# Optimization experiments

Hardware: AMD Instinct MI355X
Metric: run time of the kernel (lower is better)

Reference implementation:

```python
import jax, jax.numpy as jnp
import numpy as np

EPS = 1e-5
OFFSET_SCALE = 1.0
KPTS = 9   # 3x3 deformable kernel
GROUP = 1  # in_dim // out_dim


def _bn(x, g, b, m, v):
    # eval-mode BatchNorm2d on (B,C,H,W)
    s = g / jnp.sqrt(v + EPS)
    return x * s[None, :, None, None] + (b - m * s)[None, :, None, None]


def _dcnv4_core(value, offset, mask, offset_scale):
    # value: (B,H,W,G,Cg); offset: (B,H,W,G,K,2) as (dx,dy); mask: (B,H,W,G,K)
    B, H, W, G, Cg = value.shape
    K = mask.shape[-1]
    dt = value.dtype
    ky = jnp.repeat(jnp.arange(3) - 1, 3).astype(dt)
    kx = jnp.tile(jnp.arange(3) - 1, 3).astype(dt)
    grid = jnp.stack([kx, ky], -1)                                   # (K,2)
    base = jnp.stack(jnp.meshgrid(jnp.arange(W, dtype=dt),
                                  jnp.arange(H, dtype=dt),
                                  indexing='xy'), -1)                # (H,W,2) = (x,y)
    loc = base[None, :, :, None, None, :] + (grid + offset) * offset_scale  # (B,H,W,G,K,2)
    px, py = loc[..., 0], loc[..., 1]
    x0 = jnp.floor(px); y0 = jnp.floor(py)
    fx = px - x0; fy = py - y0
    vflat = value.transpose(0, 3, 1, 2, 4).reshape(B, G, H * W, Cg)
    out = jnp.zeros((B, G, H * W, Cg), dt)
    corners = ((0.0, 0.0, (1 - fx) * (1 - fy)), (1.0, 0.0, fx * (1 - fy)),
               (0.0, 1.0, (1 - fx) * fy), (1.0, 1.0, fx * fy))
    for dx, dy, wgt in corners:
        xi = x0 + dx; yi = y0 + dy
        valid = ((xi >= 0) & (xi < W) & (yi >= 0) & (yi < H)).astype(dt)
        idx = (jnp.clip(yi, 0, W and H - 1) * W + jnp.clip(xi, 0, W - 1)).astype(jnp.int32)
        idx = idx.transpose(0, 3, 1, 2, 4).reshape(B, G, H * W * K)
        v = jnp.take_along_axis(vflat, idx[..., None], axis=2).reshape(B, G, H * W, K, Cg)
        w = (wgt * valid * mask).transpose(0, 3, 1, 2, 4).reshape(B, G, H * W, K)
        out = out + jnp.einsum('bgsk,bgskc->bgsc', w, v)
    return out.reshape(B, G, H, W, Cg).transpose(0, 2, 3, 1, 4).reshape(B, H, W, G * Cg)


def setup_inputs() -> dict:
    key = jax.random.key(0)
    B, C, H, W = 8, 128, 64, 64
    C_OUT = 128
    OM = ((GROUP * KPTS * 3 + 7) // 8) * 8  # 32, offset_mask padded width
    ks = jax.random.split(key, 16)
    f = jnp.float32
    sc = 1.0 / np.sqrt(C).astype(np.float32)
    return {
        'x': jax.random.normal(ks[0], (B, C, H, W), f),
        'bn1_g': jax.random.uniform(ks[1], (C,), f, 0.5, 1.5),
        'bn1_b': jax.random.normal(ks[2], (C,), f) * 0.1,
        'bn1_m': jax.random.normal(ks[3], (C,), f) * 0.1,
        'bn1_v': jax.random.uniform(ks[4], (C,), f, 0.5, 1.5),
        'w_pw0': jax.random.normal(ks[5], (C, C), f) * sc,
        'w_vp': jax.random.normal(ks[6], (C, C), f) * sc,
        'b_vp': jnp.zeros((C,), f),
        'w_om': jax.random.normal(ks[7], (C, OM), f) * 0.01,
        'b_om': jnp.zeros((OM,), f),
        'w_op': jax.random.normal(ks[8], (C, C), f) * sc,
        'bn2_g': jax.random.uniform(ks[9], (C,), f, 0.5, 1.5),
        'bn2_b': jax.random.normal(ks[10], (C,), f) * 0.1,
        'bn2_m': jax.random.normal(ks[11], (C,), f) * 0.1,
        'bn2_v': jax.random.uniform(ks[12], (C,), f, 0.5, 1.5),
        'w_pw1': jax.random.normal(ks[13], (C_OUT, C), f) * sc,
    }


def reference(x, bn1_g, bn1_b, bn1_m, bn1_v, w_pw0, w_vp, b_vp, w_om, b_om, w_op,
              bn2_g, bn2_b, bn2_m, bn2_v, w_pw1):
    x = _bn(x, bn1_g, bn1_b, bn1_m, bn1_v)
    x = jnp.einsum('bchw,oc->bohw', x, w_pw0)
    B, C, H, W = x.shape
    x = x.reshape(B, H * W, C)  # raw reshape (faithful to torch .reshape, NOT a permute)
    G, K = GROUP, KPTS
    Cg = C // G
    value = (x @ w_vp + b_vp).reshape(B, H, W, G, Cg)
    om = (x @ w_om + b_om)[..., :G * K * 3].reshape(B, H, W, G, K, 3)
    out = _dcnv4_core(value, om[..., :2], om[..., 2], OFFSET_SCALE)
    out = out.reshape(B, H * W, C) @ w_op
    x = out.reshape(B, C, H, W)  # raw reshape back
    x = _bn(x, bn2_g, bn2_b, bn2_m, bn2_v)
    x = jnp.einsum('bchw,oc->bohw', x, w_pw1)
    return x
```

## Files before the change

### kernel.cpp

```cpp
#include <hip/hip_runtime.h>

#define HW 4096
#define PADU 136
typedef unsigned short ushort;
typedef __attribute__((ext_vector_type(8))) short short8;
typedef __attribute__((ext_vector_type(4))) float f32x4;

__device__ __forceinline__ ushort bf_rne(float f) {
  unsigned u = __float_as_uint(f);
  unsigned r = (u + 0x7fffu + ((u >> 16) & 1u)) >> 16;
  return (ushort)r;
}
__device__ __forceinline__ void split2(float f, ushort& hi, ushort& lo) {
  ushort h = bf_rne(f);
  float hf = __uint_as_float((unsigned)h << 16);
  hi = h;
  lo = bf_rne(f - hf);
}

__global__ __launch_bounds__(256) void prep(
    const float* __restrict__ g1, const float* __restrict__ be1,
    const float* __restrict__ m1, const float* __restrict__ v1,
    const float* __restrict__ w0,
    const float* __restrict__ g2, const float* __restrict__ be2,
    const float* __restrict__ m2, const float* __restrict__ v2,
    const float* __restrict__ w1,
    const float* __restrict__ wvp, const float* __restrict__ wom,
    const float* __restrict__ wop,
    ushort* __restrict__ W0h, ushort* __restrict__ W0l, float* __restrict__ b0,
    ushort* __restrict__ W1h, ushort* __restrict__ W1l, float* __restrict__ b1,
    ushort* __restrict__ vph, ushort* __restrict__ vpl,
    ushort* __restrict__ oph, ushort* __restrict__ opl,
    ushort* __restrict__ omh, ushort* __restrict__ oml)
{
  const int t = threadIdx.x;
// ... 35 lines not shown
      #pragma unroll
      for (int j = 0; j < 16; ++j) s += part[t >> 4][j];
      bb[o] = s;
    }
  } else if (role < 32) {
    const int rr = role & 7;
    const float* srcM = (role < 24) ? wvp : wop;
    ushort* dh = (role < 24) ? vph : oph;
    ushort* dl = (role < 24) ? vpl : opl;
    const int n = (rr << 4) + (t >> 4);
    const int kl = t & 15;
    #pragma unroll
    for (int j = 0; j < 8; ++j) {
      const int k = (kl << 3) + j;
      ushort hi, lo;
      split2(srcM[k * 128 + n], hi, lo);
      dh[n * 128 + k] = hi;
      dl[n * 128 + k] = lo;
    }
  } else {
    const int n = ((role - 32) << 4) + (t >> 4);
    const int kl = t & 15;
    #pragma unroll
    for (int j = 0; j < 8; ++j) {
      const int k = (kl << 3) + j;
      ushort hi, lo;
      split2(wom[k * 32 + n], hi, lo);
      omh[n * 128 + k] = hi;
      oml[n * 128 + k] = lo;
    }
  }
}

__global__ __launch_bounds__(512, 2) void fused_x_valom(
    const float* __restrict__ x,
    const ushort* __restrict__ W0h, const ushort* __restrict__ W0l,
    const float* __restrict__ b0,
    const ushort* __restrict__ vph, const ushort* __restrict__ vpl,
    const float* __restrict__ bvp, const float* __restrict__ bom,
    float* __restrict__ value, float* __restrict__ omb)
{
  __shared__ __align__(16) char smem[151552];
  __shared__ float b0_s[128], b2_s[160];
  ushort (*Wh_s)[128][32] = (ushort(*)[128][32])(smem);
  ushort (*Wl_s)[128][32] = (ushort(*)[128][32])(smem + 32768);
  float  (*Xf)[128][33]   = (float(*)[128][33])(smem + 65536);
  ushort (*Yh)[PADU]      = (ushort(*)[PADU])(smem);
  ushort (*Yl)[PADU]      = (ushort(*)[PADU])(smem + 34816);
  ushort (*Vh_s)[160][32] = (ushort(*)[160][32])(smem + 69632);
  ushort (*Vl_s)[160][32] = (ushort(*)[160][32])(smem + 110592);

  const int t = threadIdx.x;
  const int cb = blockIdx.x;
  const int b = blockIdx.y;
  const int hwBase = cb << 7;
  const size_t xbase = (size_t)b * (size_t)(128 * HW);
  if (t < 128) b0_s[t] = b0[t];
  if (t < 160) b2_s[t] = (t < 128) ? bvp[t] : bom[t - 128];
  const int lane = t & 63, w = t >> 6;
  const int col = lane & 15, quad = lane >> 4;
  const f32x4 z = {0.f, 0.f, 0.f, 0.f};

  uint4 vregH[5], vregL[5];
  #pragma unroll
  for (int ii = 0; ii < 5; ++ii) {
    const int i = (ii << 9) + t;
    const int kc = i / 640;
    const int r2 = i - kc * 640;
    const int n = r2 >> 2, q8 = (r2 & 3) << 3;
    vregH[ii] = *(const uint4*)&vph[n * 128 + (kc << 5) + q8];
    vregL[ii] = *(const uint4*)&vpl[n * 128 + (kc << 5) + q8];
  }

  {
    const int o = t >> 2, q8 = (t & 3) << 3;
    #pragma unroll
    for (int kc = 0; kc < 4; ++kc) {
      *(uint4*)&Wh_s[kc][o][q8] = *(const uint4*)&W0h[o * 128 + (kc << 5) + q8];
      *(uint4*)&Wl_s[kc][o][q8] = *(const uint4*)&W0l[o * 128 + (kc << 5) + q8];
    }
  }
  {
    float4 xr4[8];
    #pragma unroll
    for (int i = 0; i < 8; ++i) {
      const int idx8 = (i << 9) + t;
      xr4[i] = *(const float4*)&x[xbase + (size_t)(idx8 >> 5) * HW + hwBase + ((idx8 & 31) << 2)];
    }
    #pragma unroll
    for (int i = 0; i < 8; ++i) {
      const int idx8 = (i << 9) + t;
      const int ch = idx8 >> 5, j4 = (idx8 & 31) << 2;
      Xf[ch >> 5][j4 + 0][ch & 31] = xr4[i].x;
      Xf[ch >> 5][j4 + 1][ch & 31] = xr4[i].y;
      Xf[ch >> 5][j4 + 2][ch & 31] = xr4[i].z;
      Xf[ch >> 5][j4 + 3][ch & 31] = xr4[i].w;
    }
  }
  __syncthreads();

  f32x4 acc1[8];
  #pragma unroll
  for (int f = 0; f < 8; ++f) acc1[f] = z;

  #pragma unroll 1
  for (int kc = 0; kc < 4; ++kc) {
    union { ushort u[8]; short8 v; } bh, bl;
    {
      const float* xr = Xf[kc][(w << 4) + col] + (quad << 3);
      #pragma unroll
      for (int j = 0; j < 8; ++j) split2(xr[j], bh.u[j], bl.u[j]);
    }
    #pragma unroll
    for (int f = 0; f < 8; ++f) {
      const int row = (f << 4) + col;
      const short8 aH = *(const short8*)&Wh_s[kc][row][quad << 3];
      const short8 aL = *(const short8*)&Wl_s[kc][row][quad << 3];
      acc1[f] = __builtin_amdgcn_mfma_f32_16x16x32_bf16(aH, bh.v, acc1[f], 0, 0, 0);
      acc1[f] = __builtin_amdgcn_mfma_f32_16x16x32_bf16(aH, bl.v, acc1[f], 0, 0, 0);
      acc1[f] = __builtin_amdgcn_mfma_f32_16x16x32_bf16(aL, bh.v, acc1[f], 0, 0, 0);
    }
  }
  __syncthreads();

  #pragma unroll
  for (int ii = 0; ii < 5; ++ii) {
    const int i = (ii << 9) + t;
    const int kc = i / 640;
    const int r2 = i - kc * 640;
    const int n = r2 >> 2, q8 = (r2 & 3) << 3;
    *(uint4*)&Vh_s[kc][n][q8] = vregH[ii];
    *(uint4*)&Vl_s[kc][n][q8] = vregL[ii];
  }
  #pragma unroll
  for (int f = 0; f < 8; ++f)
    #pragma unroll
    for (int r = 0; r < 4; ++r) {
      const int o = (f << 4) + (quad << 2) + r;
      const int j = (w << 4) + col;
      ushort hi, lo;
      split2(acc1[f][r] + b0_s[o], hi, lo);
      Yh[o][j] = hi;
      Yl[o][j] = lo;
    }
  __syncthreads();

  const int wm2 = (w & 3) << 5;
  const int wn2 = (w >> 2) * 80;
  f32x4 acc2[2][5];
  #pragma unroll
  for (int i = 0; i < 2; ++i)
    #pragma unroll
    for (int j = 0; j < 5; ++j) acc2[i][j] = z;

  #pragma unroll 1
  for (int j2 = 0; j2 < 4; ++j2) {
    short8 aH[2], aL[2];
    #pragma unroll
    for (int f2 = 0; f2 < 2; ++f2) {
      const int row = wm2 + (f2 << 4) + col;
      aH[f2] = *(const short8*)&Yh[row][(j2 << 5) + (quad << 3)];
      aL[f2] = *(const short8*)&Yl[row][(j2 << 5) + (quad << 3)];
    }
    #pragma unroll
    for (int g2 = 0; g2 < 5; ++g2) {
      const int n = wn2 + (g2 << 4) + col;
      const short8 vh = *(const short8*)&Vh_s[j2][n][quad << 3];
      const short8 vl = *(const short8*)&Vl_s[j2][n][quad << 3];
      #pragma unroll
      for (int f2 = 0; f2 < 2; ++f2) {
        acc2[f2][g2] = __builtin_amdgcn_mfma_f32_16x16x32_bf16(aH[f2], vh, acc2[f2][g2], 0, 0, 0);
        acc2[f2][g2] = __builtin_amdgcn_mfma_f32_16x16x32_bf16(aH[f2], vl, acc2[f2][g2], 0, 0, 0);
        acc2[f2][g2] = __builtin_amdgcn_mfma_f32_16x16x32_bf16(aL[f2], vh, acc2[f2][g2], 0, 0, 0);
      }
    }
  }
  #pragma unroll
  for (int f2 = 0; f2 < 2; ++f2)
    #pragma unroll
    for (int r = 0; r < 4; ++r) {
      const int m = wm2 + (f2 << 4) + (quad << 2) + r;
      const size_t gRow = (size_t)b * HW + (size_t)m * 32 + cb;
      #pragma unroll
      for (int g2 = 0; g2 < 5; ++g2) {
        const int n = wn2 + (g2 << 4) + col;
        const float v = acc2[f2][g2][r] + b2_s[n];
        if (n < 128) value[gRow * 128 + n] = v;
        else         omb[gRow * 32 + (n - 128)] = v;
      }
    }
}

__global__ __launch_bounds__(512, 2) void fused_sample_op_out(
    const float* __restrict__ value, const float* __restrict__ omb,
    const ushort* __restrict__ oph, const ushort* __restrict__ opl,
    const ushort* __restrict__ W1h, const ushort* __restrict__ W1l,
    const float* __restrict__ b1, float* __restrict__ out)
{
  __shared__ __align__(16) char smem[147456];
  __shared__ float b1_s[128];
  ushort (*Afh)[128][32]  = (ushort(*)[128][32])(smem);
  ushort (*Afl)[128][32]  = (ushort(*)[128][32])(smem + 32768);
  ushort (*Bh)[128][32]   = (ushort(*)[128][32])(smem + 65536);
  ushort (*Bl)[128][32]   = (ushort(*)[128][32])(smem + 98304);
  float  (*oms)[32]       = (float(*)[32])(smem + 131072);
  ushort (*Yh)[PADU]      = (ushort(*)[PADU])(smem);
  ushort (*Yl)[PADU]      = (ushort(*)[PADU])(smem + 34816);
  ushort (*W1h_)[128][32] = (ushort(*)[128][32])(smem + 69632);
  ushort (*W1l_)[128][32] = (ushort(*)[128][32])(smem + 102400);

  const int t = threadIdx.x;
  const int blk = blockIdx.x;
  const int b = blk & 7;
  const int cb = blk >> 3;
  if (t < 128) b1_s[t] = b1[t];
  const int lane = t & 63, w = t >> 6;
  const int col = lane & 15, quad = lane >> 4;
  const f32x4 z = {0.f, 0.f, 0.f, 0.f};

  {
    const int m0 = t >> 2, j8 = (t & 3) << 3;
    const size_t orow = ((size_t)b * HW + m0 * 32 + cb) * 32;
    *(float4*)&oms[m0][j8]     = *(const float4*)&omb[orow + j8];
    *(float4*)&oms[m0][j8 + 4] = *(const float4*)&omb[orow + j8 + 4];
  }
  #pragma unroll
  for (int i = 0; i < 4; ++i) {
    const int idx = (i << 9) + t;
    const int kc = idx >> 9, n = (idx >> 2) & 127, q8 = (idx & 3) << 3;
    *(uint4*)&Bh[kc][n][q8] = *(const uint4*)&oph[n * 128 + (kc << 5) + q8];
    *(uint4*)&Bl[kc][n][q8] = *(const uint4*)&opl[n * 128 + (kc << 5) + q8];
  }
  __syncthreads();

  {
    const int xhalf = lane >> 5;
    const int c4 = (lane & 31) << 2;
    const float* vb = value + (size_t)b * (size_t)(HW * 128) + c4;
    const int kcw = (lane & 31) >> 3;
    const int cow = (lane & 7) << 2;
    #pragma unroll 1
    for (int tt = 0; tt < 16; ++tt) {
      const int m = (w << 4) + tt;
      const int s = m * 32 + cb;
      const float fw = (float)(s & 63), fh = (float)(s >> 6);
      const float* omp = oms[m];
      float a0 = 0.f, a1 = 0.f, a2 = 0.f, a3 = 0.f;
      #pragma unroll
      for (int k = 0; k < 9; ++k) {
        const float dx = omp[k * 3 + 0];
        const float dy = omp[k * 3 + 1];
        const float mw = omp[k * 3 + 2];
        const float px = fw + (float)(k % 3 - 1) + dx;
        const float py = fh + (float)(k / 3 - 1) + dy;
        const float x0f = floorf(px), y0f = floorf(py);
        const float fx = px - x0f, fy = py - y0f;
        const int ix = (int)x0f + xhalf;
        const int iy = (int)y0f;
        const float wxm = (xhalf ? fx : 1.f - fx) * mw *
                          ((ix >= 0 && ix < 64) ? 1.f : 0.f);
        const int xc = min(max(ix, 0), 63);
        const int yc0 = min(max(iy, 0), 63);
        const int yc1 = min(max(iy + 1, 0), 63);
        const float w0 = wxm * (1.f - fy) * ((iy >= 0 && iy < 64) ? 1.f : 0.f);
        const float w1 = wxm * fy * ((iy + 1 >= 0 && iy + 1 < 64) ? 1.f : 0.f);
        const float4 v0 = *(const float4*)&vb[(size_t)((yc0 << 6) + xc) * 128];
        const float4 v1 = *(const float4*)&vb[(size_t)((yc1 << 6) + xc) * 128];
        a0 = fmaf(w0, v0.x, a0); a1 = fmaf(w0, v0.y, a1);
        a2 = fmaf(w0, v0.z, a2); a3 = fmaf(w0, v0.w, a3);
        a0 = fmaf(w1, v1.x, a0); a1 = fmaf(w1, v1.y, a1);
        a2 = fmaf(w1, v1.z, a2); a3 = fmaf(w1, v1.w, a3);
      }
      a0 += __shfl_xor(a0, 32); a1 += __shfl_xor(a1, 32);
      a2 += __shfl_xor(a2, 32); a3 += __shfl_xor(a3, 32);
      if (!xhalf) {
        ushort h0, l0, h1, l1, h2, l2, h3, l3;
        split2(a0, h0, l0); split2(a1, h1, l1);
        split2(a2, h2, l2); split2(a3, h3, l3);
        uint2 uh, ul;
        uh.x = (unsigned)h0 | ((unsigned)h1 << 16);
        uh.y = (unsigned)h2 | ((unsigned)h3 << 16);
        ul.x = (unsigned)l0 | ((unsigned)l1 << 16);
        ul.y = (unsigned)l2 | ((unsigned)l3 << 16);
        *(uint2*)&Afh[kcw][m][cow] = uh;
        *(uint2*)&Afl[kcw][m][cow] = ul;
      }
    }
  }
  __syncthreads();

  const int wm1 = (w & 1) << 6, wn1 = (w >> 1) << 5;
  f32x4 acc1[4][2];
  #pragma unroll
  for (int i = 0; i < 4; ++i) { acc1[i][0] = z; acc1[i][1] = z; }

  #pragma unroll 1
  for (int kc = 0; kc < 4; ++kc) {
    short8 aH[4], aL[4];
    #pragma unroll
    for (int f = 0; f < 4; ++f) {
      const int row = wm1 + (f << 4) + col;
      aH[f] = *(const short8*)&Afh[kc][row][quad << 3];
      aL[f] = *(const short8*)&Afl[kc][row][quad << 3];
    }
    #pragma unroll
    for (int g = 0; g < 2; ++g) {
      const int n = wn1 + (g << 4) + col;
      const short8 bh = *(const short8*)&Bh[kc][n][quad << 3];
      const short8 bl = *(const short8*)&Bl[kc][n][quad << 3];
      #pragma unroll
      for (int f = 0; f < 4; ++f) {
        acc1[f][g] = __builtin_amdgcn_mfma_f32_16x16x32_bf16(aH[f], bh, acc1[f][g], 0, 0, 0);
        acc1[f][g] = __builtin_amdgcn_mfma_f32_16x16x32_bf16(aH[f], bl, acc1[f][g], 0, 0, 0);
        acc1[f][g] = __builtin_amdgcn_mfma_f32_16x16x32_bf16(aL[f], bh, acc1[f][g], 0, 0, 0);
      }
    }
  }
  __syncthreads();

  #pragma unroll
  for (int i = 0; i < 4; ++i) {
    const int n = t >> 2, q8 = (t & 3) << 3;
    *(uint4*)&W1h_[i][n][q8] = *(const uint4*)&W1h[n * 128 + (i << 5) + q8];
    *(uint4*)&W1l_[i][n][q8] = *(const uint4*)&W1l[n * 128 + (i << 5) + q8];
  }
  #pragma unroll
  for (int f = 0; f < 4; ++f)
    #pragma unroll
    for (int g = 0; g < 2; ++g)
      #pragma unroll
      for (int r = 0; r < 4; ++r) {
        const int ch = wm1 + (f << 4) + (quad << 2) + r;
        const int j  = wn1 + (g << 4) + col;
        ushort hi, lo;
        split2(acc1[f][g][r], hi, lo);
        Yh[j][ch] = hi;
        Yl[j][ch] = lo;
      }
  __syncthreads();

  const int wm2 = (w & 1) << 6, wn2 = (w >> 1) << 5;
  f32x4 acc2[4][2];
  #pragma unroll
  for (int i = 0; i < 4; ++i) { acc2[i][0] = z; acc2[i][1] = z; }

  #pragma unroll 1
  for (int j2 = 0; j2 < 4; ++j2) {
    short8 aH[4], aL[4];
    #pragma unroll
    for (int f2 = 0; f2 < 4; ++f2) {
      const int row = wm2 + (f2 << 4) + col;
      aH[f2] = *(const short8*)&W1h_[j2][row][quad << 3];
      aL[f2] = *(const short8*)&W1l_[j2][row][quad << 3];
    }
    #pragma unroll
    for (int g2 = 0; g2 < 2; ++g2) {
      const int j = wn2 + (g2 << 4) + col;
      const short8 bh = *(const short8*)&Yh[j][(j2 << 5) + (quad << 3)];
      const short8 bl = *(const short8*)&Yl[j][(j2 << 5) + (quad << 3)];
      #pragma unroll
      for (int f2 = 0; f2 < 4; ++f2) {
        acc2[f2][g2] = __builtin_amdgcn_mfma_f32_16x16x32_bf16(aH[f2], bh, acc2[f2][g2], 0, 0, 0);
        acc2[f2][g2] = __builtin_amdgcn_mfma_f32_16x16x32_bf16(aH[f2], bl, acc2[f2][g2], 0, 0, 0);
        acc2[f2][g2] = __builtin_amdgcn_mfma_f32_16x16x32_bf16(aL[f2], bh, acc2[f2][g2], 0, 0, 0);
      }
    }
  }
  const size_t obase = (size_t)b * (size_t)(128 * HW) + ((size_t)cb << 7);
  #pragma unroll
  for (int f2 = 0; f2 < 4; ++f2)
    #pragma unroll
    for (int r = 0; r < 4; ++r) {
      const int o = wm2 + (f2 << 4) + (quad << 2) + r;
      #pragma unroll
      for (int g2 = 0; g2 < 2; ++g2) {
        const int j = wn2 + (g2 << 4) + col;
        out[obase + (size_t)o * HW + j] = acc2[f2][g2][r] + b1_s[o];
      }
    }
}

extern "C" void kernel_launch(void* const* d_in, const int* in_sizes, int n_in,
                              void* d_out, int out_size, void* d_ws, size_t ws_size,
                              hipStream_t stream)
{
  const float* x    = (const float*)d_in[0];
  const float* g1   = (const float*)d_in[1];
  const float* be1  = (const float*)d_in[2];
  const float* m1   = (const float*)d_in[3];
  const float* v1   = (const float*)d_in[4];
  const float* wpw0 = (const float*)d_in[5];
  const float* wvp  = (const float*)d_in[6];
  const float* bvp  = (const float*)d_in[7];
  const float* womW = (const float*)d_in[8];
  const float* bom  = (const float*)d_in[9];
  const float* wop  = (const float*)d_in[10];
  const float* g2   = (const float*)d_in[11];
  const float* be2  = (const float*)d_in[12];
  const float* m2   = (const float*)d_in[13];
  const float* v2   = (const float*)d_in[14];
  const float* wpw1 = (const float*)d_in[15];

  char* ws = (char*)d_ws;
  float*  value = (float*) (ws + 0);
  float*  omb   = (float*) (ws + 16777216);
  size_t o = 20971520;
  ushort* W0h = (ushort*)(ws + o); o += 32768;
  ushort* W0l = (ushort*)(ws + o); o += 32768;
  ushort* W1h = (ushort*)(ws + o); o += 32768;
  ushort* W1l = (ushort*)(ws + o); o += 32768;
  ushort* vph = (ushort*)(ws + o); o += 40960;
  ushort* vpl = (ushort*)(ws + o); o += 40960;
  ushort* oph = (ushort*)(ws + o); o += 32768;
  ushort* opl = (ushort*)(ws + o); o += 32768;
  float*  b0  = (float*)(ws + o);  o += 512;
  float*  b1  = (float*)(ws + o);
  ushort* omh = vph + 128 * 128;
  ushort* oml = vpl + 128 * 128;

  prep<<<34, 256, 0, stream>>>(g1, be1, m1, v1, wpw0, g2, be2, m2, v2, wpw1,
                               wvp, womW, wop,
                               W0h, W0l, b0, W1h, W1l, b1,
                               vph, vpl, oph, opl, omh, oml);
  fused_x_valom<<<dim3(32, 8), 512, 0, stream>>>(x, W0h, W0l, b0, vph, vpl,
                                                 bvp, bom, value, omb);
  fused_sample_op_out<<<dim3(256), 512, 0, stream>>>(value, omb, oph, opl,
                                                     W1h, W1l, b1, (float*)d_out);
}
```

Baseline: 154.2 us.

## Merge projection and sampling kernels into one cooperative launch with grid sync

```diff
diff --git a/kernel.cpp b/kernel.cpp
--- a/kernel.cpp
+++ b/kernel.cpp
@@ -1,4 +1,5 @@
 #include <hip/hip_runtime.h>
+#include <hip/hip_cooperative_groups.h>
 
 #define HW 4096
 #define PADU 136
@@ -102,352 +103,348 @@
   }
 }
 
-__global__ __launch_bounds__(512, 2) void fused_x_valom(
+__global__ __launch_bounds__(512, 2) void fused_all(
     const float* __restrict__ x,
     const ushort* __restrict__ W0h, const ushort* __restrict__ W0l,
     const float* __restrict__ b0,
     const ushort* __restrict__ vph, const ushort* __restrict__ vpl,
     const float* __restrict__ bvp, const float* __restrict__ bom,
-    float* __restrict__ value, float* __restrict__ omb)
-{
-  __shared__ __align__(16) char smem[151552];
-  __shared__ float b0_s[128], b2_s[160];
-  ushort (*Wh_s)[128][32] = (ushort(*)[128][32])(smem);
-  ushort (*Wl_s)[128][32] = (ushort(*)[128][32])(smem + 32768);
-  float  (*Xf)[128][33]   = (float(*)[128][33])(smem + 65536);
-  ushort (*Yh)[PADU]      = (ushort(*)[PADU])(smem);
-  ushort (*Yl)[PADU]      = (ushort(*)[PADU])(smem + 34816);
-  ushort (*Vh_s)[160][32] = (ushort(*)[160][32])(smem + 69632);
-  ushort (*Vl_s)[160][32] = (ushort(*)[160][32])(smem + 110592);
-
-  const int t = threadIdx.x;
-  const int cb = blockIdx.x;
-  const int b = blockIdx.y;
-  const int hwBase = cb << 7;
-  const size_t xbase = (size_t)b * (size_t)(128 * HW);
-  if (t < 128) b0_s[t] = b0[t];
-  if (t < 160) b2_s[t] = (t < 128) ? bvp[t] : bom[t - 128];
-  const int lane = t & 63, w = t >> 6;
-  const int col = lane & 15, quad = lane >> 4;
-  const f32x4 z = {0.f, 0.f, 0.f, 0.f};
-
-  uint4 vregH[5], vregL[5];
-  #pragma unroll
-  for (int ii = 0; ii < 5; ++ii) {
-    const int i = (ii << 9) + t;
-    const int kc = i / 640;
-    const int r2 = i - kc * 640;
-    const int n = r2 >> 2, q8 = (r2 & 3) << 3;
-    vregH[ii] = *(const uint4*)&vph[n * 128 + (kc << 5) + q8];
-    vregL[ii] = *(const uint4*)&vpl[n * 128 + (kc << 5) + q8];
-  }
-
-  {
-    const int o = t >> 2, q8 = (t & 3) << 3;
-    #pragma unroll
-    for (int kc = 0; kc < 4; ++kc) {
-      *(uint4*)&Wh_s[kc][o][q8] = *(const uint4*)&W0h[o * 128 + (kc << 5) + q8];
-      *(uint4*)&Wl_s[kc][o][q8] = *(const uint4*)&W0l[o * 128 + (kc << 5) + q8];
-    }
-  }
-  {
-    float4 xr4[8];
-    #pragma unroll
-    for (int i = 0; i < 8; ++i) {
-      const int idx8 = (i << 9) + t;
-      xr4[i] = *(const float4*)&x[xbase + (size_t)(idx8 >> 5) * HW + hwBase + ((idx8 & 31) << 2)];
-    }
-    #pragma unroll
-    for (int i = 0; i < 8; ++i) {
-      const int idx8 = (i << 9) + t;
-      const int ch = idx8 >> 5, j4 = (idx8 & 31) << 2;
-      Xf[ch >> 5][j4 + 0][ch & 31] = xr4[i].x;
-      Xf[ch >> 5][j4 + 1][ch & 31] = xr4[i].y;
-      Xf[ch >> 5][j4 + 2][ch & 31] = xr4[i].z;
-      Xf[ch >> 5][j4 + 3][ch & 31] = xr4[i].w;
-    }
-  }
-  __syncthreads();
-
-  f32x4 acc1[8];
-  #pragma unroll
-  for (int f = 0; f < 8; ++f) acc1[f] = z;
-
-  #pragma unroll 1
-  for (int kc = 0; kc < 4; ++kc) {
-    union { ushort u[8]; short8 v; } bh, bl;
-    {
-      const float* xr = Xf[kc][(w << 4) + col] + (quad << 3);
-      #pragma unroll
-      for (int j = 0; j < 8; ++j) split2(xr[j], bh.u[j], bl.u[j]);
-    }
-    #pragma unroll
-    for (int f = 0; f < 8; ++f) {
-      const int row = (f << 4) + col;
-      const short8 aH = *(const short8*)&Wh_s[kc][row][quad << 3];
-      const short8 aL = *(const short8*)&Wl_s[kc][row][quad << 3];
-      acc1[f] = __builtin_amdgcn_mfma_f32_16x16x32_bf16(aH, bh.v, acc1[f], 0, 0, 0);
-      acc1[f] = __builtin_amdgcn_mfma_f32_16x16x32_bf16(aH, bl.v, acc1[f], 0, 0, 0);
-      acc1[f] = __builtin_amdgcn_mfma_f32_16x16x32_bf16(aL, bh.v, acc1[f], 0, 0, 0);
-    }
-  }
-  __syncthreads();
-
-  #pragma unroll
-  for (int ii = 0; ii < 5; ++ii) {
-    const int i = (ii << 9) + t;
-    const int kc = i / 640;
-    const int r2 = i - kc * 640;
-    const int n = r2 >> 2, q8 = (r2 & 3) << 3;
-    *(uint4*)&Vh_s[kc][n][q8] = vregH[ii];
-    *(uint4*)&Vl_s[kc][n][q8] = vregL[ii];
-  }
-  #pragma unroll
-  for (int f = 0; f < 8; ++f)
-    #pragma unroll
-    for (int r = 0; r < 4; ++r) {
-      const int o = (f << 4) + (quad << 2) + r;
-      const int j = (w << 4) + col;
-      ushort hi, lo;
-      split2(acc1[f][r] + b0_s[o], hi, lo);
-      Yh[o][j] = hi;
-      Yl[o][j] = lo;
-    }
-  __syncthreads();
-
-  const int wm2 = (w & 3) << 5;
-  const int wn2 = (w >> 2) * 80;
-  f32x4 acc2[2][5];
-  #pragma unroll
-  for (int i = 0; i < 2; ++i)
-    #pragma unroll
-    for (int j = 0; j < 5; ++j) acc2[i][j] = z;
-
-  #pragma unroll 1
-  for (int j2 = 0; j2 < 4; ++j2) {
-    short8 aH[2], aL[2];
-    #pragma unroll
-    for (int f2 = 0; f2 < 2; ++f2) {
-      const int row = wm2 + (f2 << 4) + col;
-      aH[f2] = *(const short8*)&Yh[row][(j2 << 5) + (quad << 3)];
-      aL[f2] = *(const short8*)&Yl[row][(j2 << 5) + (quad << 3)];
-    }
-    #pragma unroll
-    for (int g2 = 0; g2 < 5; ++g2) {
-      const int n = wn2 + (g2 << 4) + col;
-      const short8 vh = *(const short8*)&Vh_s[j2][n][quad << 3];
-      const short8 vl = *(const short8*)&Vl_s[j2][n][quad << 3];
-      #pragma unroll
-      for (int f2 = 0; f2 < 2; ++f2) {
-        acc2[f2][g2] = __builtin_amdgcn_mfma_f32_16x16x32_bf16(aH[f2], vh, acc2[f2][g2], 0, 0, 0);
-        acc2[f2][g2] = __builtin_amdgcn_mfma_f32_16x16x32_bf16(aH[f2], vl, acc2[f2][g2], 0, 0, 0);
-        acc2[f2][g2] = __builtin_amdgcn_mfma_f32_16x16x32_bf16(aL[f2], vh, acc2[f2][g2], 0, 0, 0);
-      }
-    }
-  }
-  #pragma unroll
-  for (int f2 = 0; f2 < 2; ++f2)
-    #pragma unroll
-    for (int r = 0; r < 4; ++r) {
-      const int m = wm2 + (f2 << 4) + (quad << 2) + r;
-      const size_t gRow = (size_t)b * HW + (size_t)m * 32 + cb;
-      #pragma unroll
-      for (int g2 = 0; g2 < 5; ++g2) {
-        const int n = wn2 + (g2 << 4) + col;
-        const float v = acc2[f2][g2][r] + b2_s[n];
-        if (n < 128) value[gRow * 128 + n] = v;
-        else         omb[gRow * 32 + (n - 128)] = v;
-      }
-    }
-}
-
-__global__ __launch_bounds__(512, 2) void fused_sample_op_out(
-    const float* __restrict__ value, const float* __restrict__ omb,
+    float* __restrict__ value, float* __restrict__ omb,
     const ushort* __restrict__ oph, const ushort* __restrict__ opl,
     const ushort* __restrict__ W1h, const ushort* __restrict__ W1l,
     const float* __restrict__ b1, float* __restrict__ out)
 {
-  __shared__ __align__(16) char smem[147456];
-  __shared__ float b1_s[128];
-  ushort (*Afh)[128][32]  = (ushort(*)[128][32])(smem);
-  ushort (*Afl)[128][32]  = (ushort(*)[128][32])(smem + 32768);
-  ushort (*Bh)[128][32]   = (ushort(*)[128][32])(smem + 65536);
-  ushort (*Bl)[128][32]   = (ushort(*)[128][32])(smem + 98304);
-  float  (*oms)[32]       = (float(*)[32])(smem + 131072);
-  ushort (*Yh)[PADU]      = (ushort(*)[PADU])(smem);
-  ushort (*Yl)[PADU]      = (ushort(*)[PADU])(smem + 34816);
-  ushort (*W1h_)[128][32] = (ushort(*)[128][32])(smem + 69632);
-  ushort (*W1l_)[128][32] = (ushort(*)[128][32])(smem + 102400);
+  __shared__ __align__(16) char smem[151552];
+  __shared__ float b0_s[128], b2_s[160], b1_s[128];
 
   const int t = threadIdx.x;
   const int blk = blockIdx.x;
   const int b = blk & 7;
   const int cb = blk >> 3;
-  if (t < 128) b1_s[t] = b1[t];
   const int lane = t & 63, w = t >> 6;
   const int col = lane & 15, quad = lane >> 4;
   const f32x4 z = {0.f, 0.f, 0.f, 0.f};
 
   {
-    const int m0 = t >> 2, j8 = (t & 3) << 3;
-    const size_t orow = ((size_t)b * HW + m0 * 32 + cb) * 32;
-    *(float4*)&oms[m0][j8]     = *(const float4*)&omb[orow + j8];
-    *(float4*)&oms[m0][j8 + 4] = *(const float4*)&omb[orow + j8 + 4];
+    ushort (*Wh_s)[128][32] = (ushort(*)[128][32])(smem);
+    ushort (*Wl_s)[128][32] = (ushort(*)[128][32])(smem + 32768);
+    float  (*Xf)[128][33]   = (float(*)[128][33])(smem + 65536);
+    ushort (*Yh)[PADU]      = (ushort(*)[PADU])(smem);
+    ushort (*Yl)[PADU]      = (ushort(*)[PADU])(smem + 34816);
+    ushort (*Vh_s)[160][32] = (ushort(*)[160][32])(smem + 69632);
+    ushort (*Vl_s)[160][32] = (ushort(*)[160][32])(smem + 110592);
+
+    const int hwBase = cb << 7;
+    const size_t xbase = (size_t)b * (size_t)(128 * HW);
+    if (t < 128) b0_s[t] = b0[t];
+    if (t < 160) b2_s[t] = (t < 128) ? bvp[t] : bom[t - 128];
+    if (t < 128) b1_s[t] = b1[t];
+
+    uint4 vregH[5], vregL[5];
+    #pragma unroll
+    for (int ii = 0; ii < 5; ++ii) {
+      const int i = (ii << 9) + t;
+      const int kc = i / 640;
+      const int r2 = i - kc * 640;
+      const int n = r2 >> 2, q8 = (r2 & 3) << 3;
+      vregH[ii] = *(const uint4*)&vph[n * 128 + (kc << 5) + q8];
+      vregL[ii] = *(const uint4*)&vpl[n * 128 + (kc << 5) + q8];
+    }
+
+    {
+      const int o = t >> 2, q8 = (t & 3) << 3;
+      #pragma unroll
+      for (int kc = 0; kc < 4; ++kc) {
+        *(uint4*)&Wh_s[kc][o][q8] = *(const uint4*)&W0h[o * 128 + (kc << 5) + q8];
+        *(uint4*)&Wl_s[kc][o][q8] = *(const uint4*)&W0l[o * 128 + (kc << 5) + q8];
+      }
+    }
+    {
+      float4 xr4[8];
+      #pragma unroll
+      for (int i = 0; i < 8; ++i) {
+        const int idx8 = (i << 9) + t;
+        xr4[i] = *(const float4*)&x[xbase + (size_t)(idx8 >> 5) * HW + hwBase + ((idx8 & 31) << 2)];
+      }
+      #pragma unroll
+      for (int i = 0; i < 8; ++i) {
+        const int idx8 = (i << 9) + t;
+        const int ch = idx8 >> 5, j4 = (idx8 & 31) << 2;
+        Xf[ch >> 5][j4 + 0][ch & 31] = xr4[i].x;
+        Xf[ch >> 5][j4 + 1][ch & 31] = xr4[i].y;
+        Xf[ch >> 5][j4 + 2][ch & 31] = xr4[i].z;
+        Xf[ch >> 5][j4 + 3][ch & 31] = xr4[i].w;
+      }
+    }
+    __syncthreads();
+
+    f32x4 acc1[8];
+    #pragma unroll
+    for (int f = 0; f < 8; ++f) acc1[f] = z;
+
+    #pragma unroll 1
+    for (int kc = 0; kc < 4; ++kc) {
+      union { ushort u[8]; short8 v; } bh, bl;
+      {
+        const float* xr = Xf[kc][(w << 4) + col] + (quad << 3);
+        #pragma unroll
+        for (int j = 0; j < 8; ++j) split2(xr[j], bh.u[j], bl.u[j]);
+      }
+      #pragma unroll
+      for (int f = 0; f < 8; ++f) {
+        const int row = (f << 4) + col;
+        const short8 aH = *(const short8*)&Wh_s[kc][row][quad << 3];
+        const short8 aL = *(const short8*)&Wl_s[kc][row][quad << 3];
+        acc1[f] = __builtin_amdgcn_mfma_f32_16x16x32_bf16(aH, bh.v, acc1[f], 0, 0, 0);
+        acc1[f] = __builtin_amdgcn_mfma_f32_16x16x32_bf16(aH, bl.v, acc1[f], 0, 0, 0);
+        acc1[f] = __builtin_amdgcn_mfma_f32_16x16x32_bf16(aL, bh.v, acc1[f], 0, 0, 0);
+      }
+    }
+    __syncthreads();
+
+    #pragma unroll
+    for (int ii = 0; ii < 5; ++ii) {
+      const int i = (ii << 9) + t;
+      const int kc = i / 640;
+      const int r2 = i - kc * 640;
+      const int n = r2 >> 2, q8 = (r2 & 3) << 3;
+      *(uint4*)&Vh_s[kc][n][q8] = vregH[ii];
+      *(uint4*)&Vl_s[kc][n][q8] = vregL[ii];
+    }
+    #pragma unroll
+    for (int f = 0; f < 8; ++f)
+      #pragma unroll
+      for (int r = 0; r < 4; ++r) {
+        const int o = (f << 4) + (quad << 2) + r;
+        const int j = (w << 4) + col;
+        ushort hi, lo;
+        split2(acc1[f][r] + b0_s[o], hi, lo);
+        Yh[o][j] = hi;
+        Yl[o][j] = lo;
+      }
+    __syncthreads();
+
+    const int wm2 = (w & 3) << 5;
+    const int wn2 = (w >> 2) * 80;
+    f32x4 acc2[2][5];
+    #pragma unroll
+    for (int i = 0; i < 2; ++i)
+      #pragma unroll
+      for (int j = 0; j < 5; ++j) acc2[i][j] = z;
+
+    #pragma unroll 1
+    for (int j2 = 0; j2 < 4; ++j2) {
+      short8 aH[2], aL[2];
+      #pragma unroll
+      for (int f2 = 0; f2 < 2; ++f2) {
+        const int row = wm2 + (f2 << 4) + col;
+        aH[f2] = *(const short8*)&Yh[row][(j2 << 5) + (quad << 3)];
+        aL[f2] = *(const short8*)&Yl[row][(j2 << 5) + (quad << 3)];
+      }
+      #pragma unroll
+      for (int g2 = 0; g2 < 5; ++g2) {
+        const int n = wn2 + (g2 << 4) + col;
+        const short8 vh = *(const short8*)&Vh_s[j2][n][quad << 3];
+        const short8 vl = *(const short8*)&Vl_s[j2][n][quad << 3];
+        #pragma unroll
+        for (int f2 = 0; f2 < 2; ++f2) {
+          acc2[f2][g2] = __builtin_amdgcn_mfma_f32_16x16x32_bf16(aH[f2], vh, acc2[f2][g2], 0, 0, 0);
+          acc2[f2][g2] = __builtin_amdgcn_mfma_f32_16x16x32_bf16(aH[f2], vl, acc2[f2][g2], 0, 0, 0);
+          acc2[f2][g2] = __builtin_amdgcn_mfma_f32_16x16x32_bf16(aL[f2], vh, acc2[f2][g2], 0, 0, 0);
+        }
+      }
+    }
+    #pragma unroll
+    for (int f2 = 0; f2 < 2; ++f2)
+      #pragma unroll
+      for (int r = 0; r < 4; ++r) {
+        const int m = wm2 + (f2 << 4) + (quad << 2) + r;
+        const size_t gRow = (size_t)b * HW + (size_t)m * 32 + cb;
+        #pragma unroll
+        for (int g2 = 0; g2 < 5; ++g2) {
+          const int n = wn2 + (g2 << 4) + col;
+          const float v = acc2[f2][g2][r] + b2_s[n];
+          if (n < 128) value[gRow * 128 + n] = v;
+          else         omb[gRow * 32 + (n - 128)] = v;
+        }
+      }
   }
-  #pragma unroll
-  for (int i = 0; i < 4; ++i) {
-    const int idx = (i << 9) + t;
-    const int kc = idx >> 9, n = (idx >> 2) & 127, q8 = (idx & 3) << 3;
-    *(uint4*)&Bh[kc][n][q8] = *(const uint4*)&oph[n * 128 + (kc << 5) + q8];
-    *(uint4*)&Bl[kc][n][q8] = *(const uint4*)&opl[n * 128 + (kc << 5) + q8];
-  }
-  __syncthreads();
+
+  __threadfence();
+  cooperative_groups::this_grid().sync();
 
   {
-    const int xhalf = lane >> 5;
-    const int c4 = (lane & 31) << 2;
-    const float* vb = value + (size_t)b * (size_t)(HW * 128) + c4;
-    const int kcw = (lane & 31) >> 3;
-    const int cow = (lane & 7) << 2;
+    ushort (*Afh)[128][32]  = (ushort(*)[128][32])(smem);
+    ushort (*Afl)[128][32]  = (ushort(*)[128][32])(smem + 32768);
+    ushort (*Bh)[128][32]   = (ushort(*)[128][32])(smem + 65536);
+    ushort (*Bl)[128][32]   = (ushort(*)[128][32])(smem + 98304);
+    float  (*oms)[32]       = (float(*)[32])(smem + 131072);
+    ushort (*Yh)[PADU]      = (ushort(*)[PADU])(smem);
+    ushort (*Yl)[PADU]      = (ushort(*)[PADU])(smem + 34816);
+    ushort (*W1h_)[128][32] = (ushort(*)[128][32])(smem + 69632);
+    ushort (*W1l_)[128][32] = (ushort(*)[128][32])(smem + 102400);
+
+    {
+      const int m0 = t >> 2, j8 = (t & 3) << 3;
+      const size_t orow = ((size_t)b * HW + m0 * 32 + cb) * 32;
+      *(float4*)&oms[m0][j8]     = *(const float4*)&omb[orow + j8];
+      *(float4*)&oms[m0][j8 + 4] = *(const float4*)&omb[orow + j8 + 4];
+    }
+    #pragma unroll
+    for (int i = 0; i < 4; ++i) {
+      const int idx = (i << 9) + t;
+      const int kc = idx >> 9, n = (idx >> 2) & 127, q8 = (idx & 3) << 3;
+      *(uint4*)&Bh[kc][n][q8] = *(const uint4*)&oph[n * 128 + (kc << 5) + q8];
+      *(uint4*)&Bl[kc][n][q8] = *(const uint4*)&opl[n * 128 + (kc << 5) + q8];
+    }
+    __syncthreads();
+
+    {
+      const int xhalf = lane >> 5;
+      const int c4 = (lane & 31) << 2;
+      const float* vb = value + (size_t)b * (size_t)(HW * 128) + c4;
+      const int kcw = (lane & 31) >> 3;
+      const int cow = (lane & 7) << 2;
+      #pragma unroll 1
+      for (int tt = 0; tt < 16; ++tt) {
+        const int m = (w << 4) + tt;
+        const int s = m * 32 + cb;
+        const float fw = (float)(s & 63), fh = (float)(s >> 6);
+        const float* omp = oms[m];
+        float a0 = 0.f, a1 = 0.f, a2 = 0.f, a3 = 0.f;
+        #pragma unroll
+        for (int k = 0; k < 9; ++k) {
+          const float dx = omp[k * 3 + 0];
+          const float dy = omp[k * 3 + 1];
+          const float mw = omp[k * 3 + 2];
+          const float px = fw + (float)(k % 3 - 1) + dx;
+          const float py = fh + (float)(k / 3 - 1) + dy;
+          const float x0f = floorf(px), y0f = floorf(py);
+          const float fx = px - x0f, fy = py - y0f;
+          const int ix = (int)x0f + xhalf;
+          const int iy = (int)y0f;
+          const float wxm = (xhalf ? fx : 1.f - fx) * mw *
+                            ((ix >= 0 && ix < 64) ? 1.f : 0.f);
+          const int xc = min(max(ix, 0), 63);
+          const int yc0 = min(max(iy, 0), 63);
+          const int yc1 = min(max(iy + 1, 0), 63);
+          const float w0 = wxm * (1.f - fy) * ((iy >= 0 && iy < 64) ? 1.f : 0.f);
+          const float w1 = wxm * fy * ((iy + 1 >= 0 && iy + 1 < 64) ? 1.f : 0.f);
+          const float4 v0 = *(const float4*)&vb[(size_t)((yc0 << 6) + xc) * 128];
+          const float4 v1 = *(const float4*)&vb[(size_t)((yc1 << 6) + xc) * 128];
+          a0 = fmaf(w0, v0.x, a0); a1 = fmaf(w0, v0.y, a1);
+          a2 = fmaf(w0, v0.z, a2); a3 = fmaf(w0, v0.w, a3);
+          a0 = fmaf(w1, v1.x, a0); a1 = fmaf(w1, v1.y, a1);
+          a2 = fmaf(w1, v1.z, a2); a3 = fmaf(w1, v1.w, a3);
+        }
+        a0 += __shfl_xor(a0, 32); a1 += __shfl_xor(a1, 32);
+        a2 += __shfl_xor(a2, 32); a3 += __shfl_xor(a3, 32);
+        if (!xhalf) {
+          ushort h0, l0, h1, l1, h2, l2, h3, l3;
+          split2(a0, h0, l0); split2(a1, h1, l1);
+          split2(a2, h2, l2); split2(a3, h3, l3);
+          uint2 uh, ul;
+          uh.x = (unsigned)h0 | ((unsigned)h1 << 16);
+          uh.y = (unsigned)h2 | ((unsigned)h3 << 16);
+          ul.x = (unsigned)l0 | ((unsigned)l1 << 16);
+          ul.y = (unsigned)l2 | ((unsigned)l3 << 16);
+          *(uint2*)&Afh[kcw][m][cow] = uh;
+          *(uint2*)&Afl[kcw][m][cow] = ul;
+        }
+      }
+    }
+    __syncthreads();
+
+    const int wm1 = (w & 1) << 6, wn1 = (w >> 1) << 5;
+    f32x4 acc1[4][2];
+    #pragma unroll
+    for (int i = 0; i < 4; ++i) { acc1[i][0] = z; acc1[i][1] = z; }
+
     #pragma unroll 1
-    for (int tt = 0; tt < 16; ++tt) {
-      const int m = (w << 4) + tt;
-      const int s = m * 32 + cb;
-      const float fw = (float)(s & 63), fh = (float)(s >> 6);
-      const float* omp = oms[m];
-      float a0 = 0.f, a1 = 0.f, a2 = 0.f, a3 = 0.f;
-      #pragma unroll
-      for (int k = 0; k < 9; ++k) {
-        const float dx = omp[k * 3 + 0];
-        const float dy = omp[k * 3 + 1];
-        const float mw = omp[k * 3 + 2];
-        const float px = fw + (float)(k % 3 - 1) + dx;
-        const float py = fh + (float)(k / 3 - 1) + dy;
-        const float x0f = floorf(px), y0f = floorf(py);
-        const float fx = px - x0f, fy = py - y0f;
-        const int ix = (int)x0f + xhalf;
-        const int iy = (int)y0f;
-        const float wxm = (xhalf ? fx : 1.f - fx) * mw *
-                          ((ix >= 0 && ix < 64) ? 1.f : 0.f);
-        const int xc = min(max(ix, 0), 63);
-        const int yc0 = min(max(iy, 0), 63);
-        const int yc1 = min(max(iy + 1, 0), 63);
-        const float w0 = wxm * (1.f - fy) * ((iy >= 0 && iy < 64) ? 1.f : 0.f);
-        const float w1 = wxm * fy * ((iy + 1 >= 0 && iy + 1 < 64) ? 1.f : 0.f);
-        const float4 v0 = *(const float4*)&vb[(size_t)((yc0 << 6) + xc) * 128];
-        const float4 v1 = *(const float4*)&vb[(size_t)((yc1 << 6) + xc) * 128];
-        a0 = fmaf(w0, v0.x, a0); a1 = fmaf(w0, v0.y, a1);
-        a2 = fmaf(w0, v0.z, a2); a3 = fmaf(w0, v0.w, a3);
-        a0 = fmaf(w1, v1.x, a0); a1 = fmaf(w1, v1.y, a1);
-        a2 = fmaf(w1, v1.z, a2); a3 = fmaf(w1, v1.w, a3);
-      }
-      a0 += __shfl_xor(a0, 32); a1 += __shfl_xor(a1, 32);
-      a2 += __shfl_xor(a2, 32); a3 += __shfl_xor(a3, 32);
-      if (!xhalf) {
-        ushort h0, l0, h1, l1, h2, l2, h3, l3;
-        split2(a0, h0, l0); split2(a1, h1, l1);
-        split2(a2, h2, l2); split2(a3, h3, l3);
-        uint2 uh, ul;
-        uh.x = (unsigned)h0 | ((unsigned)h1 << 16);
-        uh.y = (unsigned)h2 | ((unsigned)h3 << 16);
-        ul.x = (unsigned)l0 | ((unsigned)l1 << 16);
-        ul.y = (unsigned)l2 | ((unsigned)l3 << 16);
-        *(uint2*)&Afh[kcw][m][cow] = uh;
-        *(uint2*)&Afl[kcw][m][cow] = ul;
-      }
-    }
-  }
-  __syncthreads();
-
-  const int wm1 = (w & 1) << 6, wn1 = (w >> 1) << 5;
-  f32x4 acc1[4][2];
-  #pragma unroll
-  for (int i = 0; i < 4; ++i) { acc1[i][0] = z; acc1[i][1] = z; }
-
-  #pragma unroll 1
-  for (int kc = 0; kc < 4; ++kc) {
-    short8 aH[4], aL[4];
-    #pragma unroll
-    for (int f = 0; f < 4; ++f) {
-      const int row = wm1 + (f << 4) + col;
-      aH[f] = *(const short8*)&Afh[kc][row][quad << 3];
-      aL[f] = *(const short8*)&Afl[kc][row][quad << 3];
-    }
-    #pragma unroll
-    for (int g = 0; g < 2; ++g) {
-      const int n = wn1 + (g << 4) + col;
-      const short8 bh = *(const short8*)&Bh[kc][n][quad << 3];
-      const short8 bl = *(const short8*)&Bl[kc][n][quad << 3];
+    for (int kc = 0; kc < 4; ++kc) {
+      short8 aH[4], aL[4];
       #pragma unroll
       for (int f = 0; f < 4; ++f) {
-        acc1[f][g] = __builtin_amdgcn_mfma_f32_16x16x32_bf16(aH[f], bh, acc1[f][g], 0, 0, 0);
-        acc1[f][g] = __builtin_amdgcn_mfma_f32_16x16x32_bf16(aH[f], bl, acc1[f][g], 0, 0, 0);
-        acc1[f][g] = __builtin_amdgcn_mfma_f32_16x16x32_bf16(aL[f], bh, acc1[f][g], 0, 0, 0);
-      }
-    }
-  }
-  __syncthreads();
-
-  #pragma unroll
-  for (int i = 0; i < 4; ++i) {
-    const int n = t >> 2, q8 = (t & 3) << 3;
-    *(uint4*)&W1h_[i][n][q8] = *(const uint4*)&W1h[n * 128 + (i << 5) + q8];
-    *(uint4*)&W1l_[i][n][q8] = *(const uint4*)&W1l[n * 128 + (i << 5) + q8];
-  }
-  #pragma unroll
-  for (int f = 0; f < 4; ++f)
-    #pragma unroll
-    for (int g = 0; g < 2; ++g)
-      #pragma unroll
-      for (int r = 0; r < 4; ++r) {
-        const int ch = wm1 + (f << 4) + (quad << 2) + r;
-        const int j  = wn1 + (g << 4) + col;
-        ushort hi, lo;
-        split2(acc1[f][g][r], hi, lo);
-        Yh[j][ch] = hi;
-        Yl[j][ch] = lo;
-      }
-  __syncthreads();
-
-  const int wm2 = (w & 1) << 6, wn2 = (w >> 1) << 5;
-  f32x4 acc2[4][2];
-  #pragma unroll
-  for (int i = 0; i < 4; ++i) { acc2[i][0] = z; acc2[i][1] = z; }
-
-  #pragma unroll 1
-  for (int j2 = 0; j2 < 4; ++j2) {
-    short8 aH[4], aL[4];
-    #pragma unroll
-    for (int f2 = 0; f2 < 4; ++f2) {
-      const int row = wm2 + (f2 << 4) + col;
-      aH[f2] = *(const short8*)&W1h_[j2][row][quad << 3];
-      aL[f2] = *(const short8*)&W1l_[j2][row][quad << 3];
-    }
-    #pragma unroll
-    for (int g2 = 0; g2 < 2; ++g2) {
-      const int j = wn2 + (g2 << 4) + col;
-      const short8 bh = *(const short8*)&Yh[j][(j2 << 5) + (quad << 3)];
-      const short8 bl = *(const short8*)&Yl[j][(j2 << 5) + (quad << 3)];
+        const int row = wm1 + (f << 4) + col;
+        aH[f] = *(const short8*)&Afh[kc][row][quad << 3];
+        aL[f] = *(const short8*)&Afl[kc][row][quad << 3];
+      }
+      #pragma unroll
+      for (int g = 0; g < 2; ++g) {
+        const int n = wn1 + (g << 4) + col;
+        const short8 bh = *(const short8*)&Bh[kc][n][quad << 3];
+        const short8 bl = *(const short8*)&Bl[kc][n][quad << 3];
+        #pragma unroll
+        for (int f = 0; f < 4; ++f) {
+          acc1[f][g] = __builtin_amdgcn_mfma_f32_16x16x32_bf16(aH[f], bh, acc1[f][g], 0, 0, 0);
+          acc1[f][g] = __builtin_amdgcn_mfma_f32_16x16x32_bf16(aH[f], bl, acc1[f][g], 0, 0, 0);
+          acc1[f][g] = __builtin_amdgcn_mfma_f32_16x16x32_bf16(aL[f], bh, acc1[f][g], 0, 0, 0);
+        }
+      }
+    }
+    __syncthreads();
+
+    #pragma unroll
+    for (int i = 0; i < 4; ++i) {
+      const int n = t >> 2, q8 = (t & 3) << 3;
+      *(uint4*)&W1h_[i][n][q8] = *(const uint4*)&W1h[n * 128 + (i << 5) + q8];
+      *(uint4*)&W1l_[i][n][q8] = *(const uint4*)&W1l[n * 128 + (i << 5) + q8];
+    }
+    #pragma unroll
+    for (int f = 0; f < 4; ++f)
+      #pragma unroll
+      for (int g = 0; g < 2; ++g)
+        #pragma unroll
+        for (int r = 0; r < 4; ++r) {
+          const int ch = wm1 + (f << 4) + (quad << 2) + r;
+          const int j  = wn1 + (g << 4) + col;
+          ushort hi, lo;
+          split2(acc1[f][g][r], hi, lo);
+          Yh[j][ch] = hi;
+          Yl[j][ch] = lo;
+        }
+    __syncthreads();
+
+    const int wm2 = (w & 1) << 6, wn2 = (w >> 1) << 5;
+    f32x4 acc2[4][2];
+    #pragma unroll
+    for (int i = 0; i < 4; ++i) { acc2[i][0] = z; acc2[i][1] = z; }
+
+    #pragma unroll 1
+    for (int j2 = 0; j2 < 4; ++j2) {
+      short8 aH[4], aL[4];
       #pragma unroll
       for (int f2 = 0; f2 < 4; ++f2) {
-        acc2[f2][g2] = __builtin_amdgcn_mfma_f32_16x16x32_bf16(aH[f2], bh, acc2[f2][g2], 0, 0, 0);
-        acc2[f2][g2] = __builtin_amdgcn_mfma_f32_16x16x32_bf16(aH[f2], bl, acc2[f2][g2], 0, 0, 0);
-        acc2[f2][g2] = __builtin_amdgcn_mfma_f32_16x16x32_bf16(aL[f2], bh, acc2[f2][g2], 0, 0, 0);
-      }
-    }
-  }
-  const size_t obase = (size_t)b * (size_t)(128 * HW) + ((size_t)cb << 7);
-  #pragma unroll
-  for (int f2 = 0; f2 < 4; ++f2)
-    #pragma unroll
-    for (int r = 0; r < 4; ++r) {
-      const int o = wm2 + (f2 << 4) + (quad << 2) + r;
+        const int row = wm2 + (f2 << 4) + col;
+        aH[f2] = *(const short8*)&W1h_[j2][row][quad << 3];
+        aL[f2] = *(const short8*)&W1l_[j2][row][quad << 3];
+      }
       #pragma unroll
       for (int g2 = 0; g2 < 2; ++g2) {
         const int j = wn2 + (g2 << 4) + col;
-        out[obase + (size_t)o * HW + j] = acc2[f2][g2][r] + b1_s[o];
-      }
-    }
+        const short8 bh = *(const short8*)&Yh[j][(j2 << 5) + (quad << 3)];
+        const short8 bl = *(const short8*)&Yl[j][(j2 << 5) + (quad << 3)];
+        #pragma unroll
+        for (int f2 = 0; f2 < 4; ++f2) {
+          acc2[f2][g2] = __builtin_amdgcn_mfma_f32_16x16x32_bf16(aH[f2], bh, acc2[f2][g2], 0, 0, 0);
+          acc2[f2][g2] = __builtin_amdgcn_mfma_f32_16x16x32_bf16(aH[f2], bl, acc2[f2][g2], 0, 0, 0);
+          acc2[f2][g2] = __builtin_amdgcn_mfma_f32_16x16x32_bf16(aL[f2], bh, acc2[f2][g2], 0, 0, 0);
+        }
+      }
+    }
+    const size_t obase = (size_t)b * (size_t)(128 * HW) + ((size_t)cb << 7);
+    #pragma unroll
+    for (int f2 = 0; f2 < 4; ++f2)
+      #pragma unroll
+      for (int r = 0; r < 4; ++r) {
+        const int o = wm2 + (f2 << 4) + (quad << 2) + r;
+        #pragma unroll
+        for (int g2 = 0; g2 < 2; ++g2) {
+          const int j = wn2 + (g2 << 4) + col;
+          out[obase + (size_t)o * HW + j] = acc2[f2][g2][r] + b1_s[o];
+        }
+      }
+  }
 }
 
 extern "C" void kernel_launch(void* const* d_in, const int* in_sizes, int n_in,
@@ -492,8 +489,15 @@
                                wvp, womW, wop,
                                W0h, W0l, b0, W1h, W1l, b1,
                                vph, vpl, oph, opl, omh, oml);
-  fused_x_valom<<<dim3(32, 8), 512, 0, stream>>>(x, W0h, W0l, b0, vph, vpl,
-                                                 bvp, bom, value, omb);
-  fused_sample_op_out<<<dim3(256), 512, 0, stream>>>(value, omb, oph, opl,
-                                                     W1h, W1l, b1, (float*)d_out);
+
+  float* outp = (float*)d_out;
+  void* args[] = {
+    (void*)&x, (void*)&W0h, (void*)&W0l, (void*)&b0,
+    (void*)&vph, (void*)&vpl, (void*)&bvp, (void*)&bom,
+    (void*)&value, (void*)&omb,
+    (void*)&oph, (void*)&opl,
+    (void*)&W1h, (void*)&W1l, (void*)&b1, (void*)&outp
+  };
+  hipLaunchCooperativeKernel(reinterpret_cast<void*>(fused_all),
+                             dim3(256), dim3(512), args, 0, stream);
 }
```

Result: slower. 281.9 us (+82.8%).

## Stream weight and input chunks per k-step to shrink shared memory footprint

Applied to the files above, without the earlier changes.

```diff
diff --git a/kernel.cpp b/kernel.cpp
--- a/kernel.cpp
+++ b/kernel.cpp
@@ -1,6 +1,7 @@
 #include <hip/hip_runtime.h>
 
 #define HW 4096
+#define PADF 33
 #define PADU 136
 typedef unsigned short ushort;
 typedef __attribute__((ext_vector_type(8))) short short8;
@@ -110,15 +111,15 @@
     const float* __restrict__ bvp, const float* __restrict__ bom,
     float* __restrict__ value, float* __restrict__ omb)
 {
-  __shared__ __align__(16) char smem[151552];
+  __shared__ __align__(16) char smem[102912];
   __shared__ float b0_s[128], b2_s[160];
-  ushort (*Wh_s)[128][32] = (ushort(*)[128][32])(smem);
-  ushort (*Wl_s)[128][32] = (ushort(*)[128][32])(smem + 32768);
-  float  (*Xf)[128][33]   = (float(*)[128][33])(smem + 65536);
-  ushort (*Yh)[PADU]      = (ushort(*)[PADU])(smem);
-  ushort (*Yl)[PADU]      = (ushort(*)[PADU])(smem + 34816);
-  ushort (*Vh_s)[160][32] = (ushort(*)[160][32])(smem + 69632);
-  ushort (*Vl_s)[160][32] = (ushort(*)[160][32])(smem + 110592);
+  ushort (*Wh_s)[32] = (ushort(*)[32])(smem);
+  ushort (*Wl_s)[32] = (ushort(*)[32])(smem + 8192);
+  float*  Xf         = (float*)(smem + 16384);
+  ushort (*Vh_s)[32] = (ushort(*)[32])(smem);
+  ushort (*Vl_s)[32] = (ushort(*)[32])(smem + 10240);
+  ushort (*Yh)[PADU] = (ushort(*)[PADU])(smem + 33280);
+  ushort (*Yl)[PADU] = (ushort(*)[PADU])(smem + 68096);
 
   const int t = threadIdx.x;
   const int cb = blockIdx.x;
@@ -131,77 +132,46 @@
   const int col = lane & 15, quad = lane >> 4;
   const f32x4 z = {0.f, 0.f, 0.f, 0.f};
 
-  uint4 vregH[5], vregL[5];
-  #pragma unroll
-  for (int ii = 0; ii < 5; ++ii) {
-    const int i = (ii << 9) + t;
-    const int kc = i / 640;
-    const int r2 = i - kc * 640;
-    const int n = r2 >> 2, q8 = (r2 & 3) << 3;
-    vregH[ii] = *(const uint4*)&vph[n * 128 + (kc << 5) + q8];
-    vregL[ii] = *(const uint4*)&vpl[n * 128 + (kc << 5) + q8];
-  }
-
-  {
-    const int o = t >> 2, q8 = (t & 3) << 3;
-    #pragma unroll
-    for (int kc = 0; kc < 4; ++kc) {
-      *(uint4*)&Wh_s[kc][o][q8] = *(const uint4*)&W0h[o * 128 + (kc << 5) + q8];
-      *(uint4*)&Wl_s[kc][o][q8] = *(const uint4*)&W0l[o * 128 + (kc << 5) + q8];
-    }
-  }
-  {
-    float4 xr4[8];
-    #pragma unroll
-    for (int i = 0; i < 8; ++i) {
-      const int idx8 = (i << 9) + t;
-      xr4[i] = *(const float4*)&x[xbase + (size_t)(idx8 >> 5) * HW + hwBase + ((idx8 & 31) << 2)];
-    }
-    #pragma unroll
-    for (int i = 0; i < 8; ++i) {
-      const int idx8 = (i << 9) + t;
-      const int ch = idx8 >> 5, j4 = (idx8 & 31) << 2;
-      Xf[ch >> 5][j4 + 0][ch & 31] = xr4[i].x;
-      Xf[ch >> 5][j4 + 1][ch & 31] = xr4[i].y;
-      Xf[ch >> 5][j4 + 2][ch & 31] = xr4[i].z;
-      Xf[ch >> 5][j4 + 3][ch & 31] = xr4[i].w;
-    }
-  }
-  __syncthreads();
-
   f32x4 acc1[8];
   #pragma unroll
   for (int f = 0; f < 8; ++f) acc1[f] = z;
 
-  #pragma unroll 1
   for (int kc = 0; kc < 4; ++kc) {
+    const int kB = kc << 5;
+    {
+      const int o = t >> 2, q8 = (t & 3) << 3;
+      *(uint4*)&Wh_s[o][q8] = *(const uint4*)&W0h[o * 128 + kB + q8];
+      *(uint4*)&Wl_s[o][q8] = *(const uint4*)&W0l[o * 128 + kB + q8];
+    }
+    #pragma unroll
+    for (int p = 0; p < 2; ++p) {
+      const int idx = (p << 9) + t;
+      const int c = idx >> 5, j4 = (idx & 31) << 2;
+      const float4 f = *(const float4*)&x[xbase + (size_t)(kB + c) * HW + hwBase + j4];
+      Xf[(j4 + 0) * PADF + c] = f.x;
+      Xf[(j4 + 1) * PADF + c] = f.y;
+      Xf[(j4 + 2) * PADF + c] = f.z;
+      Xf[(j4 + 3) * PADF + c] = f.w;
+    }
+    __syncthreads();
     union { ushort u[8]; short8 v; } bh, bl;
     {
-      const float* xr = Xf[kc][(w << 4) + col] + (quad << 3);
+      const float* xr = &Xf[((w << 4) + col) * PADF + (quad << 3)];
       #pragma unroll
       for (int j = 0; j < 8; ++j) split2(xr[j], bh.u[j], bl.u[j]);
     }
     #pragma unroll
     for (int f = 0; f < 8; ++f) {
       const int row = (f << 4) + col;
-      const short8 aH = *(const short8*)&Wh_s[kc][row][quad << 3];
-      const short8 aL = *(const short8*)&Wl_s[kc][row][quad << 3];
+      const short8 aH = *(const short8*)&Wh_s[row][quad << 3];
+      const short8 aL = *(const short8*)&Wl_s[row][quad << 3];
       acc1[f] = __builtin_amdgcn_mfma_f32_16x16x32_bf16(aH, bh.v, acc1[f], 0, 0, 0);
       acc1[f] = __builtin_amdgcn_mfma_f32_16x16x32_bf16(aH, bl.v, acc1[f], 0, 0, 0);
       acc1[f] = __builtin_amdgcn_mfma_f32_16x16x32_bf16(aL, bh.v, acc1[f], 0, 0, 0);
     }
-  }
-  __syncthreads();
-
-  #pragma unroll
-  for (int ii = 0; ii < 5; ++ii) {
-    const int i = (ii << 9) + t;
-    const int kc = i / 640;
-    const int r2 = i - kc * 640;
-    const int n = r2 >> 2, q8 = (r2 & 3) << 3;
-    *(uint4*)&Vh_s[kc][n][q8] = vregH[ii];
-    *(uint4*)&Vl_s[kc][n][q8] = vregL[ii];
-  }
+    __syncthreads();
+  }
+
   #pragma unroll
   for (int f = 0; f < 8; ++f)
     #pragma unroll
@@ -213,7 +183,6 @@
       Yh[o][j] = hi;
       Yl[o][j] = lo;
     }
-  __syncthreads();
 
   const int wm2 = (w & 3) << 5;
   const int wn2 = (w >> 2) * 80;
@@ -223,8 +192,13 @@
     #pragma unroll
     for (int j = 0; j < 5; ++j) acc2[i][j] = z;
 
-  #pragma unroll 1
   for (int j2 = 0; j2 < 4; ++j2) {
+    for (int i = t; i < 640; i += 512) {
+      const int n = i >> 2, q8 = (i & 3) << 3;
+      *(uint4*)&Vh_s[n][q8] = *(const uint4*)&vph[n * 128 + (j2 << 5) + q8];
+      *(uint4*)&Vl_s[n][q8] = *(const uint4*)&vpl[n * 128 + (j2 << 5) + q8];
+    }
+    __syncthreads();
     short8 aH[2], aL[2];
     #pragma unroll
     for (int f2 = 0; f2 < 2; ++f2) {
@@ -235,8 +209,8 @@
     #pragma unroll
     for (int g2 = 0; g2 < 5; ++g2) {
       const int n = wn2 + (g2 << 4) + col;
-      const short8 vh = *(const short8*)&Vh_s[j2][n][quad << 3];
-      const short8 vl = *(const short8*)&Vl_s[j2][n][quad << 3];
+      const short8 vh = *(const short8*)&Vh_s[n][quad << 3];
+      const short8 vl = *(const short8*)&Vl_s[n][quad << 3];
       #pragma unroll
       for (int f2 = 0; f2 < 2; ++f2) {
         acc2[f2][g2] = __builtin_amdgcn_mfma_f32_16x16x32_bf16(aH[f2], vh, acc2[f2][g2], 0, 0, 0);
@@ -244,6 +218,7 @@
         acc2[f2][g2] = __builtin_amdgcn_mfma_f32_16x16x32_bf16(aL[f2], vh, acc2[f2][g2], 0, 0, 0);
       }
     }
+    __syncthreads();
   }
   #pragma unroll
   for (int f2 = 0; f2 < 2; ++f2)
```

Measured after the change: 148.1 us. -4.0%, faster.
